# Optimization experiments

Hardware: AMD Instinct MI355X
Metric: run time of the kernel (lower is better)

Reference implementation:

```python
import jax, jax.numpy as jnp
import numpy as np

TOP_K = 2  # MoE top-k routing


def setup_inputs() -> dict:
    key = jax.random.key(0)
    ks = jax.random.split(key, 5)
    B, D, H, O, N = 8192, 3072, 128, 10, 8
    scale_g = 1.0 / np.sqrt(D)
    return {
        "x": jax.random.normal(ks[0], (B, D), dtype=jnp.float32),
        "Wg": jax.random.normal(ks[1], (D, N), dtype=jnp.float32) * scale_g,
        "bg": jnp.zeros((N,), dtype=jnp.float32),
        "W1": jax.random.normal(ks[2], (N, D, H), dtype=jnp.float32) * scale_g,
        "b1": jnp.zeros((N, H), dtype=jnp.float32),
        "W2": jax.random.normal(ks[3], (N, H, O), dtype=jnp.float32) * (1.0 / np.sqrt(H)),
        "b2": jnp.zeros((N, O), dtype=jnp.float32),
    }


def reference(x, Wg, bg, W1, b1, W2, b2):
    # Gating: logits -> top-k -> softmax over the k selected logits
    g = x @ Wg + bg                                  # [B, N]
    tv, ti = jax.lax.top_k(g, TOP_K)                 # [B, k]
    w = jax.nn.softmax(tv, axis=-1)                  # [B, k]
    # Expert MLPs, computed densely over all experts (vectorized dispatch)
    h = jax.nn.relu(jnp.einsum('bd,edh->beh', x, W1) + b1)   # [B, N, H]
    y = jnp.einsum('beh,eho->beo', h, W2) + b2               # [B, N, O]
    # Combine: gather each token's k selected expert outputs, weight, sum
    ysel = jnp.take_along_axis(y, ti[:, :, None], axis=1)    # [B, k, O]
    return jnp.sum(w[:, :, None] * ysel, axis=1)             # [B, O]
```

## Files before the change

kernel.cpp:

```cpp
#include <hip/hip_runtime.h>
#include <hip/hip_bf16.h>

#define B_TOK 8192
#define D_DIM 3072
#define H_DIM 128
#define O_DIM 10
#define N_EXP 8

#define BM 128
#define BK2 128
#define HLDS_STRIDE 136
#define CHK 768
#define NCHK 4
#define ESTRIDE 4096

typedef __bf16 bf16x8 __attribute__((ext_vector_type(8)));
typedef float  f32x4  __attribute__((ext_vector_type(4)));
typedef unsigned short us8 __attribute__((ext_vector_type(8)));

__device__ __forceinline__ unsigned short f2bf(float f) {
  unsigned int u = __float_as_uint(f);
  unsigned int r = (u + 0x7FFFu + ((u >> 16) & 1u)) >> 16;
  return (unsigned short)r;
}

__device__ __forceinline__ void async16(const void* g, void* l) {
  __builtin_amdgcn_global_load_lds(
      (const __attribute__((address_space(1))) void*)g,
      (__attribute__((address_space(3))) void*)l,
      16, 0, 0);
}

__global__ __launch_bounds__(256) void k0_w1_transpose(const float* __restrict__ W1,
                                                       unsigned short* __restrict__ w1t) {
  __shared__ __align__(16) unsigned short lds[64 * 72];
  const int e  = blockIdx.z;
  const int d0 = blockIdx.x * 64;
  const int h0 = blockIdx.y * 64;
  const int tid = threadIdx.x;

  const float* src = W1 + ((size_t)e * D_DIM + d0) * H_DIM + h0;
  const int hl = tid & 63;
  const int dg = tid >> 6;
#pragma unroll
  for (int k = 0; k < 16; ++k) {
    const int d = dg + 4 * k;
    lds[hl * 72 + d] = f2bf(src[(size_t)d * H_DIM + hl]);
  }
  __syncthreads();

  unsigned short* dst = w1t + ((size_t)e * H_DIM + h0) * D_DIM + d0;
  const int q  = tid & 7;
  const int h1 = tid >> 3;
#pragma unroll
  for (int k = 0; k < 2; ++k) {
    const int h = h1 + 32 * k;
    const int d = q * 8;
    us8 v = *(const us8*)(lds + h * 72 + d);
    *(us8*)(dst + (size_t)h * D_DIM + d) = v;
  }
}

__global__ __launch_bounds__(256) void k1a_stream(
    const float* __restrict__ x, const float* __restrict__ Wg,
    unsigned short* __restrict__ xb, float* __restrict__ gpart) {
  __shared__ float wg_lds[N_EXP * CHK];
  const int c   = blockIdx.y;
  const int d0  = c * CHK;
  const int tid = threadIdx.x;

  for (int f = tid; f < CHK * N_EXP / 4; f += 256) {
    const float4 v = ((const float4*)(Wg + (size_t)d0 * N_EXP))[f];
    const int dl = f >> 1;
    const int nh = (f & 1) * 4;
    wg_lds[(nh + 0) * CHK + dl] = v.x;
    wg_lds[(nh + 1) * CHK + dl] = v.y;
    wg_lds[(nh + 2) * CHK + dl] = v.z;
    wg_lds[(nh + 3) * CHK + dl] = v.w;
  }
  __syncthreads();

  const int lane = tid & 63;
  const int wv   = tid >> 6;
  const int t0   = blockIdx.x * 16 + wv * 4;

  const float* xr0 = x + (size_t)(t0 + 0) * D_DIM + d0;
  const float* xr1 = x + (size_t)(t0 + 1) * D_DIM + d0;
  const float* xr2 = x + (size_t)(t0 + 2) * D_DIM + d0;
  const float* xr3 = x + (size_t)(t0 + 3) * D_DIM + d0;
  unsigned short* xw0 = xb + (size_t)(t0 + 0) * D_DIM + d0;
  unsigned short* xw1 = xb + (size_t)(t0 + 1) * D_DIM + d0;
  unsigned short* xw2 = xb + (size_t)(t0 + 2) * D_DIM + d0;
  unsigned short* xw3 = xb + (size_t)(t0 + 3) * D_DIM + d0;

  float acc[4][N_EXP];
#pragma unroll
  for (int t = 0; t < 4; ++t)
#pragma unroll
    for (int n = 0; n < N_EXP; ++n) acc[t][n] = 0.f;

#pragma unroll
  for (int s = 0; s < CHK / 256; ++s) {
    const int dl = s * 256 + lane * 4;
    float4 xv0 = *(const float4*)(xr0 + dl);
    float4 xv1 = *(const float4*)(xr1 + dl);
    float4 xv2 = *(const float4*)(xr2 + dl);
    float4 xv3 = *(const float4*)(xr3 + dl);
    float4 w4[N_EXP];
#pragma unroll
    for (int n = 0; n < N_EXP; ++n)
      w4[n] = *(const float4*)(wg_lds + n * CHK + dl);
    ushort4 p;
    p.x = f2bf(xv0.x); p.y = f2bf(xv0.y); p.z = f2bf(xv0.z); p.w = f2bf(xv0.w);
    *(ushort4*)(xw0 + dl) = p;
    p.x = f2bf(xv1.x); p.y = f2bf(xv1.y); p.z = f2bf(xv1.z); p.w = f2bf(xv1.w);
    *(ushort4*)(xw1 + dl) = p;
    p.x = f2bf(xv2.x); p.y = f2bf(xv2.y); p.z = f2bf(xv2.z); p.w = f2bf(xv2.w);
    *(ushort4*)(xw2 + dl) = p;
    p.x = f2bf(xv3.x); p.y = f2bf(xv3.y); p.z = f2bf(xv3.z); p.w = f2bf(xv3.w);
    *(ushort4*)(xw3 + dl) = p;
#pragma unroll
    for (int n = 0; n < N_EXP; ++n) {
      acc[0][n] = fmaf(xv0.x, w4[n].x, acc[0][n]);
      acc[0][n] = fmaf(xv0.y, w4[n].y, acc[0][n]);
      acc[0][n] = fmaf(xv0.z, w4[n].z, acc[0][n]);
      acc[0][n] = fmaf(xv0.w, w4[n].w, acc[0][n]);
      acc[1][n] = fmaf(xv1.x, w4[n].x, acc[1][n]);
      acc[1][n] = fmaf(xv1.y, w4[n].y, acc[1][n]);
      acc[1][n] = fmaf(xv1.z, w4[n].z, acc[1][n]);
      acc[1][n] = fmaf(xv1.w, w4[n].w, acc[1][n]);
      acc[2][n] = fmaf(xv2.x, w4[n].x, acc[2][n]);
      acc[2][n] = fmaf(xv2.y, w4[n].y, acc[2][n]);
      acc[2][n] = fmaf(xv2.z, w4[n].z, acc[2][n]);
      acc[2][n] = fmaf(xv2.w, w4[n].w, acc[2][n]);
      acc[3][n] = fmaf(xv3.x, w4[n].x, acc[3][n]);
      acc[3][n] = fmaf(xv3.y, w4[n].y, acc[3][n]);
      acc[3][n] = fmaf(xv3.z, w4[n].z, acc[3][n]);
      acc[3][n] = fmaf(xv3.w, w4[n].w, acc[3][n]);
    }
  }

#pragma unroll
  for (int t = 0; t < 4; ++t)
#pragma unroll
    for (int n = 0; n < N_EXP; ++n) {
#pragma unroll
      for (int off = 32; off > 0; off >>= 1)
        acc[t][n] += __shfl_xor(acc[t][n], off, 64);
    }
  if (lane == 0) {
#pragma unroll
    for (int t = 0; t < 4; ++t) {
      float* gp = gpart + ((size_t)c * B_TOK + (t0 + t)) * N_EXP;
      *(float4*)(gp)     = make_float4(acc[t][0], acc[t][1], acc[t][2], acc[t][3]);
      *(float4*)(gp + 4) = make_float4(acc[t][4], acc[t][5], acc[t][6], acc[t][7]);
    }
  }
}

__global__ __launch_bounds__(256) void k1c_topk(
    const float* __restrict__ gpart, const float* __restrict__ bg,
    int4* __restrict__ idx4, float2* __restrict__ wts, int* __restrict__ cnt,
    int* __restrict__ tlist) {
  __shared__ int lcnt[N_EXP], gbase[N_EXP];
  __shared__ float bgs[N_EXP];
  const int tid = threadIdx.x;
  if (tid < N_EXP) { lcnt[tid] = 0; bgs[tid] = bg[tid]; }
  __syncthreads();
  const int t = blockIdx.x * 256 + tid;

  float g[N_EXP];
#pragma unroll
  for (int n = 0; n < N_EXP; ++n) g[n] = bgs[n];
#pragma unroll
  for (int c = 0; c < NCHK; ++c) {
    const float* gp = gpart + ((size_t)c * B_TOK + t) * N_EXP;
    float4 a = *(const float4*)(gp);
    float4 b = *(const float4*)(gp + 4);
    g[0] += a.x; g[1] += a.y; g[2] += a.z; g[3] += a.w;
    g[4] += b.x; g[5] += b.y; g[6] += b.z; g[7] += b.w;
  }
  int i0 = 0;
#pragma unroll
  for (int n = 1; n < N_EXP; ++n) if (g[n] > g[i0]) i0 = n;
  int i1 = (i0 == 0) ? 1 : 0;
#pragma unroll
  for (int n = 0; n < N_EXP; ++n) if (n != i0 && g[n] > g[i1]) i1 = n;
  const float e1 = expf(g[i1] - g[i0]);
  const float inv = 1.f / (1.f + e1);
  const int lp0 = atomicAdd(&lcnt[i0], 1);
  const int lp1 = atomicAdd(&lcnt[i1], 1);
  __syncthreads();
  if (tid < N_EXP) gbase[tid] = atomicAdd(&cnt[tid], lcnt[tid]);
  __syncthreads();
  int p0 = gbase[i0] + lp0; p0 = p0 < ESTRIDE ? p0 : ESTRIDE - 1;
  int p1 = gbase[i1] + lp1; p1 = p1 < ESTRIDE ? p1 : ESTRIDE - 1;
  tlist[i0 * ESTRIDE + p0] = t;
  tlist[i1 * ESTRIDE + p1] = t;
  idx4[t] = make_int4(i0, p0, i1, p1);
  wts[t]  = make_float2(inv, e1 * inv);
}

__global__ __launch_bounds__(256) void k2_experts(
    const unsigned short* __restrict__ xb,
    const unsigned short* __restrict__ w1t,
    const float* __restrict__ b1,
    const float* __restrict__ W2,
    const float* __restrict__ b2,
    const int* __restrict__ cnt, const int* __restrict__ tlist,
    float* __restrict__ ypair) {
  const int e    = blockIdx.y;
  int n_e        = cnt[e];
  n_e            = n_e < ESTRIDE ? n_e : ESTRIDE;
  const int row0 = blockIdx.x * BM;
  if (row0 >= n_e) return;

  __shared__ __align__(16) unsigned short sm[65536 + 2048];
  unsigned short* h_lds   = sm;
  unsigned short* w2t_lds = sm + 65536;

  const int tid  = threadIdx.x;
  const int lane = tid & 63;
  const int wv   = tid >> 6;
  const int quad = lane >> 4;
  const int cl   = lane & 15;

  const unsigned short* Abase[8];
  const unsigned short* Bbase[8];
#pragma unroll
  for (int j = 0; j < 8; ++j) {
    const int rloc = wv * 32 + j * 4 + quad;
    int gr = row0 + rloc;
    gr = gr < n_e ? gr : n_e - 1;
    const int koff = ((cl - (j * 4 + quad)) & 15) * 8;
    Abase[j] = xb + (size_t)tlist[e * ESTRIDE + gr] * D_DIM + koff;
    Bbase[j] = w1t + ((size_t)e * H_DIM + rloc) * D_DIM + koff;
  }

#define STAGE(it, pp)                                                     \
  {                                                                       \
    const int ko = (it) * BK2;                                            \
    unsigned short* abuf = sm + (pp) * 32768;                             \
    unsigned short* bbuf = sm + 16384 + (pp) * 32768;                     \
    _Pragma("unroll")                                                     \
    for (int j = 0; j < 8; ++j) {                                         \
      const int ldsrow = (wv * 32 + j * 4) * BK2;                         \
      async16(Abase[j] + ko, abuf + ldsrow);                              \
      async16(Bbase[j] + ko, bbuf + ldsrow);                              \
    }                                                                     \
  }

  STAGE(0, 0);

  const float* W2e = W2 + (size_t)e * H_DIM * O_DIM;
  for (int idx = tid; idx < 16 * 128; idx += 256) {
    const int o = idx >> 7, hh = idx & 127;
    const float v = (o < O_DIM) ? W2e[hh * O_DIM + o] : 0.f;
    w2t_lds[o * 128 + ((((hh >> 3) + o) & 15) * 8) + (hh & 7)] = f2bf(v);
  }

  const int mhalf = (wv >> 1) * 64;
  const int nhalf = (wv & 1) * 64;

  f32x4 acc[4][4];
#pragma unroll
  for (int i = 0; i < 4; ++i)
#pragma unroll
    for (int j = 0; j < 4; ++j)
      acc[i][j] = (f32x4){0.f, 0.f, 0.f, 0.f};

  const int NIT = D_DIM / BK2;
  for (int it = 0; it < NIT; ++it) {
    __syncthreads();
    if (it + 1 < NIT) STAGE(it + 1, (it + 1) & 1);
    const unsigned short* al = sm + (it & 1) * 32768;
    const unsigned short* bl = sm + 16384 + (it & 1) * 32768;
#pragma unroll
    for (int kk = 0; kk < 4; ++kk) {
      const int pos = ((kk * 4 + quad + cl) & 15) * 8;
      bf16x8 af[4], bfr[4];
#pragma unroll
      for (int mi = 0; mi < 4; ++mi)
        af[mi] = *(const bf16x8*)(al + (mhalf + mi * 16 + cl) * BK2 + pos);
#pragma unroll
      for (int ni = 0; ni < 4; ++ni)
        bfr[ni] = *(const bf16x8*)(bl + (nhalf + ni * 16 + cl) * BK2 + pos);
#pragma unroll
      for (int mi = 0; mi < 4; ++mi)
#pragma unroll
        for (int ni = 0; ni < 4; ++ni)
          acc[mi][ni] = __builtin_amdgcn_mfma_f32_16x16x32_bf16(af[mi], bfr[ni], acc[mi][ni], 0, 0, 0);
    }
  }
  __syncthreads();

  const float* b1e = b1 + e * H_DIM;
#pragma unroll
  for (int ni = 0; ni < 4; ++ni) {
    const int col  = nhalf + ni * 16 + cl;
    const float bias = b1e[col];
#pragma unroll
    for (int mi = 0; mi < 4; ++mi) {
      const int rbase = mhalf + mi * 16 + (quad << 2);
#pragma unroll
      for (int r = 0; r < 4; ++r) {
        float v = acc[mi][ni][r] + bias;
        v = v > 0.f ? v : 0.f;
        h_lds[(rbase + r) * HLDS_STRIDE + col] = f2bf(v);
      }
    }
  }
  __syncthreads();

  f32x4 acc2[2];
  acc2[0] = (f32x4){0.f, 0.f, 0.f, 0.f};
  acc2[1] = (f32x4){0.f, 0.f, 0.f, 0.f};
#pragma unroll
  for (int ks = 0; ks < 4; ++ks) {
    const int krd = ks * 32 + quad * 8;
    bf16x8 bfr = *(const bf16x8*)(w2t_lds + cl * 128 + ((ks * 4 + quad + cl) & 15) * 8);
#pragma unroll
    for (int mi = 0; mi < 2; ++mi) {
      bf16x8 afr = *(const bf16x8*)(h_lds + (wv * 32 + mi * 16 + cl) * HLDS_STRIDE + krd);
      acc2[mi] = __builtin_amdgcn_mfma_f32_16x16x32_bf16(afr, bfr, acc2[mi], 0, 0, 0);
    }
  }
  const int o = cl;
  if (o < O_DIM) {
    const float bias2 = b2[e * O_DIM + o];
#pragma unroll
    for (int mi = 0; mi < 2; ++mi) {
#pragma unroll
      for (int r = 0; r < 4; ++r) {
        const int rl = wv * 32 + mi * 16 + (quad << 2) + r;
        if (row0 + rl < n_e)
          ypair[(size_t)(e * ESTRIDE + row0 + rl) * 16 + o] = acc2[mi][r] + bias2;
      }
    }
  }
}

__global__ __launch_bounds__(256) void k3_combine(
    const float* __restrict__ ypair, const int4* __restrict__ idx4,
    const float2* __restrict__ wts, float* __restrict__ out) {
  const int g = blockIdx.x * 256 + threadIdx.x;
  if (g >= B_TOK * O_DIM) return;
  const int b = g / O_DIM, o = g - b * O_DIM;
  const int4 r = idx4[b];
  const float2 w = wts[b];
  out[g] = w.x * ypair[(size_t)(r.x * ESTRIDE + r.y) * 16 + o] +
           w.y * ypair[(size_t)(r.z * ESTRIDE + r.w) * 16 + o];
}

extern "C" void kernel_launch(void* const* d_in, const int* in_sizes, int n_in,
                              void* d_out, int out_size, void* d_ws, size_t ws_size,
                              hipStream_t stream) {
  const float* x  = (const float*)d_in[0];
  const float* Wg = (const float*)d_in[1];
  const float* bg = (const float*)d_in[2];
  const float* W1 = (const float*)d_in[3];
  const float* b1 = (const float*)d_in[4];
  const float* W2 = (const float*)d_in[5];
  const float* b2 = (const float*)d_in[6];
  float* out = (float*)d_out;

  char* ws = (char*)d_ws;
  unsigned short* xb  = (unsigned short*)ws;
  unsigned short* w1t = (unsigned short*)(ws + 50331648);
  int4*   idx4  = (int4*)  (ws + 56623104);
  float2* wts   = (float2*)(ws + 56754176);
  int*    cnt   = (int*)   (ws + 56819712);
  int*    tlist = (int*)   (ws + 56819840);
  float*  gpart = (float*) (ws + 56950912);
  float*  ypair = (float*) (ws + 56950912);

  k0_w1_transpose<<<dim3(48, 2, 8), dim3(256), 0, stream>>>(W1, w1t);
  (void)hipMemsetAsync(cnt, 0, N_EXP * sizeof(int), stream);
  k1a_stream<<<dim3(B_TOK / 16, NCHK), dim3(256), 0, stream>>>(x, Wg, xb, gpart);
  k1c_topk<<<dim3(B_TOK / 256), dim3(256), 0, stream>>>(gpart, bg, idx4, wts, cnt, tlist);
  k2_experts<<<dim3(ESTRIDE / BM, N_EXP), dim3(256), 0, stream>>>(
      xb, w1t, b1, W2, b2, cnt, tlist, ypair);
  k3_combine<<<dim3((B_TOK * O_DIM + 255) / 256), dim3(256), 0, stream>>>(
      ypair, idx4, wts, out);
}
```

Before: 235.2 us.

## Drop bf16 x staging buffer; convert fp32 x in-register inside expert GEMM

The gate kernel no longer writes a bf16 copy of x. It processes 8 tokens per wave and uses a transposed shuffle reduction so every lane writes one gate logit. The expert kernel now loads gathered fp32 x rows directly into registers, packs them to bf16 and writes them to LDS after the MFMA loop, which overlaps the global loads with compute. M tile shrinks from 128 to 64 rows to reduce LDS use and launch more blocks. This removes the 48MB bf16 write and reread, but doubles per-row fp32 read traffic in the expert GEMM, adds register pressure, and uses a simpler round-half-up conversion.

```diff
diff --git a/kernel.cpp b/kernel.cpp
--- a/kernel.cpp
+++ b/kernel.cpp
@@ -7,7 +7,7 @@
 #define O_DIM 10
 #define N_EXP 8
 
-#define BM 128
+#define BM2 64
 #define BK2 128
 #define HLDS_STRIDE 136
 #define CHK 768
@@ -22,6 +22,12 @@
   unsigned int u = __float_as_uint(f);
   unsigned int r = (u + 0x7FFFu + ((u >> 16) & 1u)) >> 16;
   return (unsigned short)r;
+}
+
+__device__ __forceinline__ unsigned int pk2(float a, float b) {
+  unsigned int ua = (__float_as_uint(a) + 0x8000u) >> 16;
+  unsigned int ub = (__float_as_uint(b) + 0x8000u) & 0xFFFF0000u;
+  return ub | ua;
 }
 
 __device__ __forceinline__ void async16(const void* g, void* l) {
@@ -61,9 +67,9 @@
   }
 }
 
-__global__ __launch_bounds__(256) void k1a_stream(
+__global__ __launch_bounds__(256) void k1a_gate(
     const float* __restrict__ x, const float* __restrict__ Wg,
-    unsigned short* __restrict__ xb, float* __restrict__ gpart) {
+    float* __restrict__ gpart) {
   __shared__ float wg_lds[N_EXP * CHK];
   const int c   = blockIdx.y;
   const int d0  = c * CHK;
@@ -71,8 +77,8 @@
 
   for (int f = tid; f < CHK * N_EXP / 4; f += 256) {
     const float4 v = ((const float4*)(Wg + (size_t)d0 * N_EXP))[f];
-    const int dl = f >> 1;
-    const int nh = (f & 1) * 4;
+    const int dl  = f >> 1;
+    const int nh  = (f & 1) * 4;
     wg_lds[(nh + 0) * CHK + dl] = v.x;
     wg_lds[(nh + 1) * CHK + dl] = v.y;
     wg_lds[(nh + 2) * CHK + dl] = v.z;
@@ -82,80 +88,58 @@
 
   const int lane = tid & 63;
   const int wv   = tid >> 6;
-  const int t0   = blockIdx.x * 16 + wv * 4;
-
-  const float* xr0 = x + (size_t)(t0 + 0) * D_DIM + d0;
-  const float* xr1 = x + (size_t)(t0 + 1) * D_DIM + d0;
-  const float* xr2 = x + (size_t)(t0 + 2) * D_DIM + d0;
-  const float* xr3 = x + (size_t)(t0 + 3) * D_DIM + d0;
-  unsigned short* xw0 = xb + (size_t)(t0 + 0) * D_DIM + d0;
-  unsigned short* xw1 = xb + (size_t)(t0 + 1) * D_DIM + d0;
-  unsigned short* xw2 = xb + (size_t)(t0 + 2) * D_DIM + d0;
-  unsigned short* xw3 = xb + (size_t)(t0 + 3) * D_DIM + d0;
-
-  float acc[4][N_EXP];
-#pragma unroll
-  for (int t = 0; t < 4; ++t)
+  const int t0   = blockIdx.x * 32 + wv * 8;
+  const float* xr = x + (size_t)t0 * D_DIM + d0;
+
+  float acc[8][N_EXP];
+#pragma unroll
+  for (int t = 0; t < 8; ++t)
 #pragma unroll
     for (int n = 0; n < N_EXP; ++n) acc[t][n] = 0.f;
 
 #pragma unroll
   for (int s = 0; s < CHK / 256; ++s) {
     const int dl = s * 256 + lane * 4;
-    float4 xv0 = *(const float4*)(xr0 + dl);
-    float4 xv1 = *(const float4*)(xr1 + dl);
-    float4 xv2 = *(const float4*)(xr2 + dl);
-    float4 xv3 = *(const float4*)(xr3 + dl);
     float4 w4[N_EXP];
 #pragma unroll
     for (int n = 0; n < N_EXP; ++n)
       w4[n] = *(const float4*)(wg_lds + n * CHK + dl);
-    ushort4 p;
-    p.x = f2bf(xv0.x); p.y = f2bf(xv0.y); p.z = f2bf(xv0.z); p.w = f2bf(xv0.w);
-    *(ushort4*)(xw0 + dl) = p;
-    p.x = f2bf(xv1.x); p.y = f2bf(xv1.y); p.z = f2bf(xv1.z); p.w = f2bf(xv1.w);
-    *(ushort4*)(xw1 + dl) = p;
-    p.x = f2bf(xv2.x); p.y = f2bf(xv2.y); p.z = f2bf(xv2.z); p.w = f2bf(xv2.w);
-    *(ushort4*)(xw2 + dl) = p;
-    p.x = f2bf(xv3.x); p.y = f2bf(xv3.y); p.z = f2bf(xv3.z); p.w = f2bf(xv3.w);
-    *(ushort4*)(xw3 + dl) = p;
+#pragma unroll
+    for (int t = 0; t < 8; ++t) {
+      const float4 xv = *(const float4*)(xr + (size_t)t * D_DIM + dl);
+#pragma unroll
+      for (int n = 0; n < N_EXP; ++n) {
+        acc[t][n] = fmaf(xv.x, w4[n].x, acc[t][n]);
+        acc[t][n] = fmaf(xv.y, w4[n].y, acc[t][n]);
+        acc[t][n] = fmaf(xv.z, w4[n].z, acc[t][n]);
+        acc[t][n] = fmaf(xv.w, w4[n].w, acc[t][n]);
+      }
+    }
+  }
+
+  const int g  = lane >> 3;
+  const int tt = lane & 7;
+  float v[8];
+#pragma unroll
+  for (int t = 0; t < 8; ++t) {
 #pragma unroll
     for (int n = 0; n < N_EXP; ++n) {
-      acc[0][n] = fmaf(xv0.x, w4[n].x, acc[0][n]);
-      acc[0][n] = fmaf(xv0.y, w4[n].y, acc[0][n]);
-      acc[0][n] = fmaf(xv0.z, w4[n].z, acc[0][n]);
-      acc[0][n] = fmaf(xv0.w, w4[n].w, acc[0][n]);
-      acc[1][n] = fmaf(xv1.x, w4[n].x, acc[1][n]);
-      acc[1][n] = fmaf(xv1.y, w4[n].y, acc[1][n]);
-      acc[1][n] = fmaf(xv1.z, w4[n].z, acc[1][n]);
-      acc[1][n] = fmaf(xv1.w, w4[n].w, acc[1][n]);
-      acc[2][n] = fmaf(xv2.x, w4[n].x, acc[2][n]);
-      acc[2][n] = fmaf(xv2.y, w4[n].y, acc[2][n]);
-      acc[2][n] = fmaf(xv2.z, w4[n].z, acc[2][n]);
-      acc[2][n] = fmaf(xv2.w, w4[n].w, acc[2][n]);
-      acc[3][n] = fmaf(xv3.x, w4[n].x, acc[3][n]);
-      acc[3][n] = fmaf(xv3.y, w4[n].y, acc[3][n]);
-      acc[3][n] = fmaf(xv3.z, w4[n].z, acc[3][n]);
-      acc[3][n] = fmaf(xv3.w, w4[n].w, acc[3][n]);
-    }
-  }
-
-#pragma unroll
-  for (int t = 0; t < 4; ++t)
-#pragma unroll
-    for (int n = 0; n < N_EXP; ++n) {
-#pragma unroll
-      for (int off = 32; off > 0; off >>= 1)
-        acc[t][n] += __shfl_xor(acc[t][n], off, 64);
-    }
-  if (lane == 0) {
-#pragma unroll
-    for (int t = 0; t < 4; ++t) {
-      float* gp = gpart + ((size_t)c * B_TOK + (t0 + t)) * N_EXP;
-      *(float4*)(gp)     = make_float4(acc[t][0], acc[t][1], acc[t][2], acc[t][3]);
-      *(float4*)(gp + 4) = make_float4(acc[t][4], acc[t][5], acc[t][6], acc[t][7]);
-    }
-  }
+      acc[t][n] += __shfl_xor(acc[t][n], 32, 64);
+      acc[t][n] += __shfl_xor(acc[t][n], 16, 64);
+      acc[t][n] += __shfl_xor(acc[t][n], 8, 64);
+    }
+    float s = acc[t][0];
+#pragma unroll
+    for (int n = 1; n < N_EXP; ++n) s = (g == n) ? acc[t][n] : s;
+    s += __shfl_xor(s, 1, 64);
+    s += __shfl_xor(s, 2, 64);
+    s += __shfl_xor(s, 4, 64);
+    v[t] = s;
+  }
+  float out = v[0];
+#pragma unroll
+  for (int t = 1; t < 8; ++t) out = (tt == t) ? v[t] : out;
+  gpart[((size_t)c * B_TOK + t0 + tt) * N_EXP + g] = out;
 }
 
 __global__ __launch_bounds__(256) void k1c_topk(
@@ -202,7 +186,7 @@
 }
 
 __global__ __launch_bounds__(256) void k2_experts(
-    const unsigned short* __restrict__ xb,
+    const float* __restrict__ x,
     const unsigned short* __restrict__ w1t,
     const float* __restrict__ b1,
     const float* __restrict__ W2,
@@ -212,12 +196,12 @@
   const int e    = blockIdx.y;
   int n_e        = cnt[e];
   n_e            = n_e < ESTRIDE ? n_e : ESTRIDE;
-  const int row0 = blockIdx.x * BM;
+  const int row0 = blockIdx.x * BM2;
   if (row0 >= n_e) return;
 
-  __shared__ __align__(16) unsigned short sm[65536 + 2048];
+  __shared__ __align__(16) unsigned short sm[51200];
   unsigned short* h_lds   = sm;
-  unsigned short* w2t_lds = sm + 65536;
+  unsigned short* w2t_lds = sm + 49152;
 
   const int tid  = threadIdx.x;
   const int lane = tid & 63;
@@ -225,32 +209,54 @@
   const int quad = lane >> 4;
   const int cl   = lane & 15;
 
-  const unsigned short* Abase[8];
+  const float* Abase[4];
+#pragma unroll
+  for (int w = 0; w < 4; ++w) {
+    int gr = row0 + wv * 16 + w * 4 + quad;
+    gr = gr < n_e ? gr : n_e - 1;
+    Abase[w] = x + (size_t)tlist[e * ESTRIDE + gr] * D_DIM + cl * 8;
+  }
   const unsigned short* Bbase[8];
 #pragma unroll
   for (int j = 0; j < 8; ++j) {
     const int rloc = wv * 32 + j * 4 + quad;
-    int gr = row0 + rloc;
-    gr = gr < n_e ? gr : n_e - 1;
     const int koff = ((cl - (j * 4 + quad)) & 15) * 8;
-    Abase[j] = xb + (size_t)tlist[e * ESTRIDE + gr] * D_DIM + koff;
     Bbase[j] = w1t + ((size_t)e * H_DIM + rloc) * D_DIM + koff;
   }
 
-#define STAGE(it, pp)                                                     \
+  float4 av[4][2];
+
+#define STAGE_LOAD(it, pp)                                                \
   {                                                                       \
     const int ko = (it) * BK2;                                            \
-    unsigned short* abuf = sm + (pp) * 32768;                             \
-    unsigned short* bbuf = sm + 16384 + (pp) * 32768;                     \
     _Pragma("unroll")                                                     \
-    for (int j = 0; j < 8; ++j) {                                         \
-      const int ldsrow = (wv * 32 + j * 4) * BK2;                         \
-      async16(Abase[j] + ko, abuf + ldsrow);                              \
-      async16(Bbase[j] + ko, bbuf + ldsrow);                              \
+    for (int w = 0; w < 4; ++w) {                                         \
+      av[w][0] = *(const float4*)(Abase[w] + ko);                         \
+      av[w][1] = *(const float4*)(Abase[w] + ko + 4);                     \
     }                                                                     \
-  }
-
-  STAGE(0, 0);
+    unsigned short* bbuf = sm + 8192 + (pp) * 24576;                      \
+    _Pragma("unroll")                                                     \
+    for (int j = 0; j < 8; ++j)                                           \
+      async16(Bbase[j] + ko, bbuf + (wv * 32 + j * 4) * BK2);             \
+  }
+
+#define STAGE_WRITE(pp)                                                   \
+  {                                                                       \
+    unsigned short* abuf = sm + (pp) * 24576;                             \
+    _Pragma("unroll")                                                     \
+    for (int w = 0; w < 4; ++w) {                                         \
+      const int rloc = wv * 16 + w * 4 + quad;                            \
+      uint4 pk;                                                           \
+      pk.x = pk2(av[w][0].x, av[w][0].y);                                 \
+      pk.y = pk2(av[w][0].z, av[w][0].w);                                 \
+      pk.z = pk2(av[w][1].x, av[w][1].y);                                 \
+      pk.w = pk2(av[w][1].z, av[w][1].w);                                 \
+      *(uint4*)(abuf + rloc * BK2 + ((cl + rloc) & 15) * 8) = pk;         \
+    }                                                                     \
+  }
+
+  STAGE_LOAD(0, 0);
+  STAGE_WRITE(0);
 
   const float* W2e = W2 + (size_t)e * H_DIM * O_DIM;
   for (int idx = tid; idx < 16 * 128; idx += 256) {
@@ -259,12 +265,12 @@
     w2t_lds[o * 128 + ((((hh >> 3) + o) & 15) * 8) + (hh & 7)] = f2bf(v);
   }
 
-  const int mhalf = (wv >> 1) * 64;
+  const int mhalf = (wv >> 1) * 32;
   const int nhalf = (wv & 1) * 64;
 
-  f32x4 acc[4][4];
-#pragma unroll
-  for (int i = 0; i < 4; ++i)
+  f32x4 acc[2][4];
+#pragma unroll
+  for (int i = 0; i < 2; ++i)
 #pragma unroll
     for (int j = 0; j < 4; ++j)
       acc[i][j] = (f32x4){0.f, 0.f, 0.f, 0.f};
@@ -272,25 +278,27 @@
   const int NIT = D_DIM / BK2;
   for (int it = 0; it < NIT; ++it) {
     __syncthreads();
-    if (it + 1 < NIT) STAGE(it + 1, (it + 1) & 1);
-    const unsigned short* al = sm + (it & 1) * 32768;
-    const unsigned short* bl = sm + 16384 + (it & 1) * 32768;
+    const int pp = it & 1, np = pp ^ 1;
+    if (it + 1 < NIT) STAGE_LOAD(it + 1, np);
+    const unsigned short* al = sm + pp * 24576;
+    const unsigned short* bl = sm + 8192 + pp * 24576;
 #pragma unroll
     for (int kk = 0; kk < 4; ++kk) {
       const int pos = ((kk * 4 + quad + cl) & 15) * 8;
-      bf16x8 af[4], bfr[4];
-#pragma unroll
-      for (int mi = 0; mi < 4; ++mi)
+      bf16x8 af[2], bfr[4];
+#pragma unroll
+      for (int mi = 0; mi < 2; ++mi)
         af[mi] = *(const bf16x8*)(al + (mhalf + mi * 16 + cl) * BK2 + pos);
 #pragma unroll
       for (int ni = 0; ni < 4; ++ni)
         bfr[ni] = *(const bf16x8*)(bl + (nhalf + ni * 16 + cl) * BK2 + pos);
 #pragma unroll
-      for (int mi = 0; mi < 4; ++mi)
+      for (int mi = 0; mi < 2; ++mi)
 #pragma unroll
         for (int ni = 0; ni < 4; ++ni)
           acc[mi][ni] = __builtin_amdgcn_mfma_f32_16x16x32_bf16(af[mi], bfr[ni], acc[mi][ni], 0, 0, 0);
     }
+    if (it + 1 < NIT) STAGE_WRITE(np);
   }
   __syncthreads();
 
@@ -300,7 +308,7 @@
     const int col  = nhalf + ni * 16 + cl;
     const float bias = b1e[col];
 #pragma unroll
-    for (int mi = 0; mi < 4; ++mi) {
+    for (int mi = 0; mi < 2; ++mi) {
       const int rbase = mhalf + mi * 16 + (quad << 2);
 #pragma unroll
       for (int r = 0; r < 4; ++r) {
@@ -312,30 +320,22 @@
   }
   __syncthreads();
 
-  f32x4 acc2[2];
-  acc2[0] = (f32x4){0.f, 0.f, 0.f, 0.f};
-  acc2[1] = (f32x4){0.f, 0.f, 0.f, 0.f};
+  f32x4 acc2 = (f32x4){0.f, 0.f, 0.f, 0.f};
 #pragma unroll
   for (int ks = 0; ks < 4; ++ks) {
     const int krd = ks * 32 + quad * 8;
     bf16x8 bfr = *(const bf16x8*)(w2t_lds + cl * 128 + ((ks * 4 + quad + cl) & 15) * 8);
-#pragma unroll
-    for (int mi = 0; mi < 2; ++mi) {
-      bf16x8 afr = *(const bf16x8*)(h_lds + (wv * 32 + mi * 16 + cl) * HLDS_STRIDE + krd);
-      acc2[mi] = __builtin_amdgcn_mfma_f32_16x16x32_bf16(afr, bfr, acc2[mi], 0, 0, 0);
-    }
+    bf16x8 afr = *(const bf16x8*)(h_lds + (wv * 16 + cl) * HLDS_STRIDE + krd);
+    acc2 = __builtin_amdgcn_mfma_f32_16x16x32_bf16(afr, bfr, acc2, 0, 0, 0);
   }
   const int o = cl;
   if (o < O_DIM) {
     const float bias2 = b2[e * O_DIM + o];
 #pragma unroll
-    for (int mi = 0; mi < 2; ++mi) {
-#pragma unroll
-      for (int r = 0; r < 4; ++r) {
-        const int rl = wv * 32 + mi * 16 + (quad << 2) + r;
-        if (row0 + rl < n_e)
-          ypair[(size_t)(e * ESTRIDE + row0 + rl) * 16 + o] = acc2[mi][r] + bias2;
-      }
+    for (int r = 0; r < 4; ++r) {
+      const int rl = wv * 16 + (quad << 2) + r;
+      if (row0 + rl < n_e)
+        ypair[(size_t)(e * ESTRIDE + row0 + rl) * 16 + o] = acc2[r] + bias2;
     }
   }
 }
@@ -365,21 +365,20 @@
   float* out = (float*)d_out;
 
   char* ws = (char*)d_ws;
-  unsigned short* xb  = (unsigned short*)ws;
-  unsigned short* w1t = (unsigned short*)(ws + 50331648);
-  int4*   idx4  = (int4*)  (ws + 56623104);
-  float2* wts   = (float2*)(ws + 56754176);
-  int*    cnt   = (int*)   (ws + 56819712);
-  int*    tlist = (int*)   (ws + 56819840);
-  float*  gpart = (float*) (ws + 56950912);
-  float*  ypair = (float*) (ws + 56950912);
+  unsigned short* w1t = (unsigned short*)ws;
+  int4*   idx4  = (int4*)  (ws + 6291456);
+  float2* wts   = (float2*)(ws + 6422528);
+  int*    cnt   = (int*)   (ws + 6488064);
+  int*    tlist = (int*)   (ws + 6488192);
+  float*  gpart = (float*) (ws + 6619264);
+  float*  ypair = (float*) (ws + 6619264);
 
   k0_w1_transpose<<<dim3(48, 2, 8), dim3(256), 0, stream>>>(W1, w1t);
   (void)hipMemsetAsync(cnt, 0, N_EXP * sizeof(int), stream);
-  k1a_stream<<<dim3(B_TOK / 16, NCHK), dim3(256), 0, stream>>>(x, Wg, xb, gpart);
+  k1a_gate<<<dim3(B_TOK / 32, NCHK), dim3(256), 0, stream>>>(x, Wg, gpart);
   k1c_topk<<<dim3(B_TOK / 256), dim3(256), 0, stream>>>(gpart, bg, idx4, wts, cnt, tlist);
-  k2_experts<<<dim3(ESTRIDE / BM, N_EXP), dim3(256), 0, stream>>>(
-      xb, w1t, b1, W2, b2, cnt, tlist, ypair);
+  k2_experts<<<dim3(ESTRIDE / BM2, N_EXP), dim3(256), 0, stream>>>(
+      x, w1t, b1, W2, b2, cnt, tlist, ypair);
   k3_combine<<<dim3((B_TOK * O_DIM + 255) / 256), dim3(256), 0, stream>>>(
       ypair, idx4, wts, out);
 }
```

Result: slower. 267.1 us (+13.6%).
